# Kernel tuning notes

Hardware: AMD Instinct MI355X
Metric: run time of the kernel (lower is better)

Reference implementation:

```python
import jax, jax.numpy as jnp
import numpy as np

SIM_TIME = 3
ALPHA = 0.9      # membrane decay
RHO = 0.985      # threshold-adaptation decay
BETA_A = 1.8     # adaptation coupling
TH = 1.0         # base threshold
SURR_SCALE = 0.3 # surrogate gradient scale

@jax.custom_vjp
def spike(v):
    return (v > 0.0).astype(v.dtype)

def _spike_fwd(v):
    return spike(v), v

def _spike_bwd(v, g):
    # triangular surrogate gradient
    return (g * SURR_SCALE * jnp.maximum(0.0, 1.0 - jnp.abs(v)),)

spike.defvjp(_spike_fwd, _spike_bwd)

def setup_inputs() -> dict:
    key = jax.random.key(0)
    ks = jax.random.split(key, 6)
    T, B, nin, npre, nad, npost, nout = 32, 128, 512, 1024, 1024, 1024, 256
    s = lambda fan_in: 1.0 / np.sqrt(fan_in)
    return {
        "inp": jax.random.normal(ks[0], (T, B, nin), dtype=jnp.float32),
        "W_pre": jax.random.normal(ks[1], (npre, nin + nad), dtype=jnp.float32) * s(nin + nad),
        "b_pre": jnp.zeros((npre,), jnp.float32),
        "W_ad": jax.random.normal(ks[2], (nad, npre), dtype=jnp.float32) * s(npre),
        "b_ad": jnp.zeros((nad,), jnp.float32),
        "W_post": jax.random.normal(ks[3], (npost, nin + nad), dtype=jnp.float32) * s(nin + nad),
        "b_post": jnp.zeros((npost,), jnp.float32),
        "W_out": jax.random.normal(ks[4], (nout, npost), dtype=jnp.float32) * s(npost),
        "b_out": jnp.zeros((nout,), jnp.float32),
    }

def _rsnn_forward(inp, W_pre, b_pre, W_ad, b_ad, W_post, b_post, W_out, b_out):
    T, B, _ = inp.shape
    nad = W_ad.shape[0]
    npre = W_pre.shape[0]
    npost = W_post.shape[0]
    z = lambda n: jnp.zeros((B, n), inp.dtype)
    # state: (adaptive spikes, v_pre, v_adapt, b_adapt, v_post)
    init = (z(nad), z(npre), z(nad), z(nad), z(npost))

    def step_t(state, inp_t):
        spikes, v_pre, v_a, b_a, v_post = state
        o = None
        for _ in range(SIM_TIME):  # fixed small inner simulation loop
            x = jnp.concatenate([inp_t, spikes], axis=1)            # [B, nin+nad]
            v_pre = ALPHA * v_pre + x @ W_pre.T + b_pre
            s_pre = spike(v_pre - TH)
            v_pre = v_pre - s_pre * TH                               # soft reset
            v_a = ALPHA * v_a + s_pre @ W_ad.T + b_ad
            th_eff = TH + BETA_A * b_a                               # adaptive threshold
            s_a = spike(v_a - th_eff)
            v_a = v_a - s_a * th_eff
            b_a = RHO * b_a + s_a
            spikes = s_a
            x2 = jnp.concatenate([inp_t, s_a], axis=1)
            v_post = ALPHA * v_post + x2 @ W_post.T + b_post
            s_post = spike(v_post - TH)
            v_post = v_post - s_post * TH
            o = s_post @ W_out.T + b_out                             # [B, nout]
        return (spikes, v_pre, v_a, b_a, v_post), o

    final_state, output = jax.lax.scan(step_t, init, inp)            # output [T, B, nout]
    return output, final_state[0]

def reference(inp, W_pre, b_pre, W_ad, b_ad, W_post, b_post, W_out, b_out):
    return _rsnn_forward(inp, W_pre, b_pre, W_ad, b_ad, W_post, b_post, W_out, b_out)
```

## Files before the change

### kernel.cpp

```cpp
#include <hip/hip_runtime.h>

#pragma clang fp contract(off)

typedef unsigned long long u64;
typedef unsigned int u32;

#define ALPHA  0.9f
#define RHO    0.985f
#define BETA_A 1.8f
#define TH     1.0f
#define CAP    (1 << 24)

__global__ __launch_bounds__(256) void transpose_k(const float* __restrict__ src,
                                                   float* __restrict__ dst,
                                                   int R, int C) {
    __shared__ float tile[32][33];
    const int c0 = blockIdx.x * 32;
    const int r0 = blockIdx.y * 32;
    const int tx = threadIdx.x, ty = threadIdx.y;
#pragma unroll
    for (int i = 0; i < 4; ++i)
        tile[ty + i * 8][tx] = src[(r0 + ty + i * 8) * C + c0 + tx];
    __syncthreads();
#pragma unroll
    for (int i = 0; i < 4; ++i)
        dst[(c0 + ty + i * 8) * R + r0 + tx] = tile[tx][ty + i * 8];
}

__global__ __launch_bounds__(256) void ip_gemm(const float* __restrict__ inp,
                                               const float* __restrict__ Wt,
                                               const float* __restrict__ bias,
                                               float* __restrict__ out) {
    __shared__ __align__(16) float s_in[512 * 20];
    const int tid   = threadIdx.x;
    const int chunk = blockIdx.x;
    const int rbase = blockIdx.y * 16;

    for (int idx = tid; idx < 16 * 512; idx += 256) {
        const int r = idx >> 9, k = idx & 511;
        s_in[k * 20 + r] = inp[(rbase + r) * 512 + k];
    }
    __syncthreads();

    const int n = chunk * 256 + tid;
    float acc[16];
#pragma unroll
    for (int r = 0; r < 16; ++r) acc[r] = 0.f;

    for (int k = 0; k < 512; ++k) {
        const float w = Wt[k * 1024 + n];
        const float4* p = (const float4*)(s_in + k * 20);
        const float4 x0 = p[0], x1 = p[1], x2 = p[2], x3 = p[3];
        acc[0]  = fmaf(x0.x, w, acc[0]);  acc[1]  = fmaf(x0.y, w, acc[1]);
        acc[2]  = fmaf(x0.z, w, acc[2]);  acc[3]  = fmaf(x0.w, w, acc[3]);
        acc[4]  = fmaf(x1.x, w, acc[4]);  acc[5]  = fmaf(x1.y, w, acc[5]);
        acc[6]  = fmaf(x1.z, w, acc[6]);  acc[7]  = fmaf(x1.w, w, acc[7]);
        acc[8]  = fmaf(x2.x, w, acc[8]);  acc[9]  = fmaf(x2.y, w, acc[9]);
        acc[10] = fmaf(x2.z, w, acc[10]); acc[11] = fmaf(x2.w, w, acc[11]);
        acc[12] = fmaf(x3.x, w, acc[12]); acc[13] = fmaf(x3.y, w, acc[13]);
        acc[14] = fmaf(x3.z, w, acc[14]); acc[15] = fmaf(x3.w, w, acc[15]);
    }
    const float bn = bias[n];
#pragma unroll
    for (int r = 0; r < 16; ++r) out[(rbase + r) * 1024 + n] = acc[r] + bn;
}

__device__ __forceinline__ u64 ld_u64(const u64* p) {
    return __hip_atomic_load(p, __ATOMIC_RELAXED, __HIP_MEMORY_SCOPE_AGENT);
}
__device__ __forceinline__ void st_u64(u64* p, u64 v) {
    __hip_atomic_store(p, v, __ATOMIC_RELAXED, __HIP_MEMORY_SCOPE_AGENT);
}

__device__ __forceinline__ float gatherseg(const char* __restrict__ Wb,
                                           const int* __restrict__ list,
                                           int i0, int i1, int colB) {
    float a0 = 0.f, a1 = 0.f, a2 = 0.f, a3 = 0.f;
    int i = i0;
    for (; i + 4 <= i1; i += 4) {
        const int4 j = *(const int4*)(list + i);
        a0 += *(const float*)(Wb + (u32)(j.x + colB));
        a1 += *(const float*)(Wb + (u32)(j.y + colB));
        a2 += *(const float*)(Wb + (u32)(j.z + colB));
        a3 += *(const float*)(Wb + (u32)(j.w + colB));
    }
    for (; i < i1; ++i) a0 += *(const float*)(Wb + (u32)(list[i] + colB));
    return (a0 + a1) + (a2 + a3);
}

__device__ __forceinline__ float gather_idx(const float* __restrict__ W,
                                            const int* __restrict__ list, int cnt, int col) {
    float a0 = 0.f, a1 = 0.f, a2 = 0.f, a3 = 0.f;
    int i = 0;
    for (; i + 4 <= cnt; i += 4) {
        const int4 j = *(const int4*)(list + i);
        a0 += W[j.x * 256 + col];
        a1 += W[j.y * 256 + col];
        a2 += W[j.z * 256 + col];
        a3 += W[j.w * 256 + col];
    }
    for (; i < cnt; ++i) a0 += W[list[i] * 256 + col];
    return (a0 + a1) + (a2 + a3);
}

__global__ __launch_bounds__(640) void rsnn_pc(
    const float* __restrict__ Wt_pre,
    const float* __restrict__ Wt_ad,
    const float* __restrict__ Wt_post,
    const float* __restrict__ IP_pre,
    const float* __restrict__ IP_post,
    const float* __restrict__ b_ad_p,
    u64* __restrict__ lines,
    u64* __restrict__ spkO,
    float* __restrict__ out)
{
    const int tid  = threadIdx.x;
    const int bid  = blockIdx.x;
    const int x    = bid & 7;
    const int g    = bid >> 3;
    const int s    = x >> 1;
    const int p    = g * 2 + (x & 1);
    const int wid  = tid >> 6;
    const int lane = tid & 63;

    __shared__ __align__(16) int listP[2][1024];
    __shared__ __align__(16) int listS[2][2][1024];
    __shared__ int cntP_ls[2], cntS_ls[2][2];

    const char* WadB    = (const char*)Wt_ad;
    const char* WpreAB  = (const char*)(Wt_pre  + 512 * 1024);
    const char* WpostAB = (const char*)(Wt_post + 512 * 1024);

    if (wid < 8) {
        const int bi   = tid >> 8;
        const int c    = tid & 255;
        const int col  = s * 256 + c;
        const int b    = 2 * p + bi;
        const int q    = wid & 3;
        const int colB = col * 4;

        float v_pre = 0.f, v_a = 0.f, ba = 0.f, v_post = 0.f, accA = 0.f;
        bool  sa = false;
        const float bad = b_ad_p[col];
        float g1 = 0.f;
        int halfPrev = 0, cntPrev = 0, parPrev = 0;

        for (int e = 1; e <= 96; ++e) {
            const int par = e & 1;
            const int t   = (e - 1) / 3;
            const float ipre = IP_pre[(t * 128 + b) * 1024 + col];
            u64* ln0 = lines + ((p * 2 + par) * 2 + 0) * 64;
            u64* ln1 = lines + ((p * 2 + par) * 2 + 1) * 64;

            v_pre = ALPHA * v_pre + ipre + accA;
            float d = v_pre - TH;
            const bool sp = d > 0.f;
            if (sp) v_pre = d;
            {
                const u64 m = __ballot(sp);
                if (lane == 0) {
                    const u64 eh = ((u64)e) << 32;
                    st_u64(&ln0[(s * 2 + bi) * 8 + 2 * q],     eh | (m & 0xffffffffull));
                    st_u64(&ln0[(s * 2 + bi) * 8 + 2 * q + 1], eh | (m >> 32));
                }
            }
            if (e >= 2)
                g1 = gatherseg(WpostAB, listS[parPrev][bi], 0, halfPrev, colB);
            __syncthreads();

            const int cp = cntP_ls[bi];
            const float accB = gatherseg(WadB, listP[bi], 0, cp, colB);
            v_a = ALPHA * v_a + accB + bad;
            const float th = TH + BETA_A * ba;
            d = v_a - th;
            sa = d > 0.f;
            if (sa) v_a = d;
            ba = RHO * ba + (sa ? 1.f : 0.f);
            {
                const u64 m = __ballot(sa);
                if (lane == 0) {
                    const u64 eh = ((u64)e) << 32;
                    st_u64(&ln1[(s * 2 + bi) * 8 + 2 * q],     eh | (m & 0xffffffffull));
                    st_u64(&ln1[(s * 2 + bi) * 8 + 2 * q + 1], eh | (m >> 32));
                }
            }
            if (e >= 2) {
                const float g2 = gatherseg(WpostAB, listS[parPrev][bi],
                                           halfPrev, cntPrev, colB);
                const int tp = (e - 2) / 3;
                const float ipost = IP_post[(tp * 128 + b) * 1024 + col];
                v_post = ALPHA * v_post + ipost + (g1 + g2);
                float dd = v_post - TH;
                const bool spost = dd > 0.f;
                if (spost) v_post = dd;
                if (e % 3 == 1) {
                    const u64 m = __ballot(spost);
                    if (lane == 0)
                        st_u64(&spkO[(tp * 128 + 2 * p + bi) * 16 + s * 4 + q], m);
                }
            }
            if (e == 96)
                out[32 * 128 * 256 + b * 1024 + col] = sa ? 1.f : 0.f;
            __syncthreads();

            const int cs = cntS_ls[par][bi];
            halfPrev = (cs >> 1) & ~3;
            cntPrev  = cs;
            parPrev  = par;
            if (e < 96)
                accA = gatherseg(WpreAB, listS[par][bi], 0, cs, colB);
        }
        {
            const float ga = gatherseg(WpostAB, listS[0][bi], 0, halfPrev, colB);
            const float gb = gatherseg(WpostAB, listS[0][bi], halfPrev, cntPrev, colB);
            const float ipost = IP_post[(31 * 128 + b) * 1024 + col];
            v_post = ALPHA * v_post + ipost + (ga + gb);
            const float dd = v_post - TH;
            const u64 m = __ballot(dd > 0.f);
            if (lane == 0)
                st_u64(&spkO[(31 * 128 + 2 * p + bi) * 16 + s * 4 + q], m);
        }
    } else if (wid == 8) {
        const int cbi = lane >> 5, r = lane & 31, sl = r >> 3, h = r & 7;
        const int jbase = (sl * 256 + h * 32) << 12;
        for (int e = 1; e <= 96; ++e) {
            const int par = e & 1;
            const u64* ln0 = lines + ((p * 2 + par) * 2 + 0) * 64;
            u64 w; int gd = 0;
            do { w = ld_u64(&ln0[(sl * 2 + cbi) * 8 + h]); }
            while ((w >> 32) != (u64)e && ++gd < CAP);
            const u32 bits = (u32)w;
            const int pc = __popc(bits);
            int incl = pc;
            for (int dlt = 1; dlt < 32; dlt <<= 1) {
                const int v = __shfl_up(incl, dlt, 32);
                if ((lane & 31) >= dlt) incl += v;
            }
            int base = incl - pc;
            u32 m = bits;
            while (m) {
                const int bt = __builtin_ctz(m);
                m &= m - 1;
                listP[cbi][base++] = jbase + (bt << 12);
            }
            if ((lane & 31) == 31) cntP_ls[cbi] = incl;
            __syncthreads();
            __syncthreads();
        }
    } else {
        const int cbi = lane >> 5, r = lane & 31, sl = r >> 3, h = r & 7;
        const int jbase = (sl * 256 + h * 32) << 12;
        for (int e = 1; e <= 96; ++e) {
            const int par = e & 1;
            const u64* ln1 = lines + ((p * 2 + par) * 2 + 1) * 64;
            __syncthreads();
            u64 w; int gd = 0;
            do { w = ld_u64(&ln1[(sl * 2 + cbi) * 8 + h]); }
            while ((w >> 32) != (u64)e && ++gd < CAP);
            const u32 bits = (u32)w;
            const int pc = __popc(bits);
            int incl = pc;
            for (int dlt = 1; dlt < 32; dlt <<= 1) {
                const int v = __shfl_up(incl, dlt, 32);
                if ((lane & 31) >= dlt) incl += v;
            }
            int base = incl - pc;
            u32 m = bits;
            while (m) {
                const int bt = __builtin_ctz(m);
                m &= m - 1;
                listS[par][cbi][base++] = jbase + (bt << 12);
            }
            if ((lane & 31) == 31) cntS_ls[par][cbi] = incl;
            __syncthreads();
        }
    }
}

__global__ __launch_bounds__(256) void out_gemm(const float* __restrict__ Wt_out,
                                                const float* __restrict__ b_out,
                                                const u64* __restrict__ spkO,
                                                float* __restrict__ out) {
    __shared__ u64 bmp[16];
    __shared__ int pc[16];
    __shared__ __align__(16) int list[1024];
    const int r = blockIdx.x, tid = threadIdx.x;
    if (tid < 16) {
        const u64 m = ld_u64(&spkO[r * 16 + tid]);
        bmp[tid] = m;
        pc[tid]  = __popcll(m);
    }
    __syncthreads();
    int total = 0;
#pragma unroll
    for (int w = 0; w < 16; ++w) total += pc[w];
    for (int j = tid; j < 1024; j += 256) {
        const int w = j >> 6, bit = j & 63;
        const u64 m = bmp[w];
        if ((m >> bit) & 1ull) {
            int base = __popcll(m & ((1ull << bit) - 1ull));
            for (int q2 = 0; q2 < w; ++q2) base += pc[q2];
            list[base] = j;
        }
    }
    __syncthreads();
    const float acc = gather_idx(Wt_out, list, total, tid);
    out[r * 256 + tid] = acc + b_out[tid];
}

extern "C" void kernel_launch(void* const* d_in, const int* in_sizes, int n_in,
                              void* d_out, int out_size, void* d_ws, size_t ws_size,
                              hipStream_t stream) {
    (void)in_sizes; (void)n_in; (void)out_size; (void)ws_size;
    const float* inp    = (const float*)d_in[0];
    const float* W_pre  = (const float*)d_in[1];
    const float* b_pre  = (const float*)d_in[2];
    const float* W_ad   = (const float*)d_in[3];
    const float* b_ad   = (const float*)d_in[4];
    const float* W_post = (const float*)d_in[5];
    const float* b_post = (const float*)d_in[6];
    const float* W_out  = (const float*)d_in[7];
    const float* b_out  = (const float*)d_in[8];

    char* base = (char*)d_ws;
    u64*  lines = (u64*)(base + 4096);
    u64*  spkO  = (u64*)(base + 147456);
    float* ws      = (float*)(base + 1048576);
    float* Wt_pre  = ws;
    float* Wt_post = Wt_pre  + 1536 * 1024;
    float* Wt_ad   = Wt_post + 1536 * 1024;
    float* Wt_out  = Wt_ad   + 1024 * 1024;
    float* IP_pre  = Wt_out  + 1024 * 256;
    float* IP_post = IP_pre  + 4096 * 1024;

    hipMemsetAsync(base, 0, 4096 + 131072, stream);

    transpose_k<<<dim3(48, 32), dim3(32, 8), 0, stream>>>(W_pre,  Wt_pre,  1024, 1536);
    transpose_k<<<dim3(48, 32), dim3(32, 8), 0, stream>>>(W_post, Wt_post, 1024, 1536);
    transpose_k<<<dim3(32, 32), dim3(32, 8), 0, stream>>>(W_ad,   Wt_ad,   1024, 1024);
    transpose_k<<<dim3(32, 8),  dim3(32, 8), 0, stream>>>(W_out,  Wt_out,  256,  1024);

    ip_gemm<<<dim3(4, 256), 256, 0, stream>>>(inp, Wt_pre,  b_pre,  IP_pre);
    ip_gemm<<<dim3(4, 256), 256, 0, stream>>>(inp, Wt_post, b_post, IP_post);

    rsnn_pc<<<256, 640, 0, stream>>>(Wt_pre, Wt_ad, Wt_post,
                                     IP_pre, IP_post, b_ad,
                                     lines, spkO, (float*)d_out);

    out_gemm<<<4096, 256, 0, stream>>>(Wt_out, b_out, spkO, (float*)d_out);
}
```

Measured before the change: 1.084 ms.

## Split recurrent kernel to one batch row per block with merged list-builder wave

The persistent recurrent kernel now has each block handle a single batch row instead of two. That doubles the grid to 512 blocks of 320 threads. The two list-builder waves (pre spikes and adaptive spikes) are merged into one wave that handles both stages in sequence. The intent is to spread the gather work over more CUs and shrink per-block shared memory. The cost is a longer serial path in the single builder wave and twice as many spin-polling blocks, which must all be co-resident to avoid deadlock.

```diff
diff --git a/kernel.cpp b/kernel.cpp
--- a/kernel.cpp
+++ b/kernel.cpp
@@ -103,7 +103,7 @@
     return (a0 + a1) + (a2 + a3);
 }
 
-__global__ __launch_bounds__(640) void rsnn_pc(
+__global__ __launch_bounds__(320) void rsnn_pc2(
     const float* __restrict__ Wt_pre,
     const float* __restrict__ Wt_ad,
     const float* __restrict__ Wt_post,
@@ -119,24 +119,24 @@
     const int x    = bid & 7;
     const int g    = bid >> 3;
     const int s    = x >> 1;
-    const int p    = g * 2 + (x & 1);
+    const int b    = g * 2 + (x & 1);
     const int wid  = tid >> 6;
     const int lane = tid & 63;
 
-    __shared__ __align__(16) int listP[2][1024];
-    __shared__ __align__(16) int listS[2][2][1024];
-    __shared__ int cntP_ls[2], cntS_ls[2][2];
+    __shared__ __align__(16) int listP[1024];
+    __shared__ __align__(16) int listS[2][1024];
+    __shared__ int cntP_ls, cntS_ls[2];
 
     const char* WadB    = (const char*)Wt_ad;
     const char* WpreAB  = (const char*)(Wt_pre  + 512 * 1024);
     const char* WpostAB = (const char*)(Wt_post + 512 * 1024);
 
-    if (wid < 8) {
-        const int bi   = tid >> 8;
-        const int c    = tid & 255;
-        const int col  = s * 256 + c;
-        const int b    = 2 * p + bi;
-        const int q    = wid & 3;
+    if (tid == 0) { cntS_ls[0] = 0; cntS_ls[1] = 0; cntP_ls = 0; }
+    __syncthreads();
+
+    if (wid < 4) {
+        const int q    = wid;
+        const int col  = s * 256 + tid;
         const int colB = col * 4;
 
         float v_pre = 0.f, v_a = 0.f, ba = 0.f, v_post = 0.f, accA = 0.f;
@@ -149,8 +149,8 @@
             const int par = e & 1;
             const int t   = (e - 1) / 3;
             const float ipre = IP_pre[(t * 128 + b) * 1024 + col];
-            u64* ln0 = lines + ((p * 2 + par) * 2 + 0) * 64;
-            u64* ln1 = lines + ((p * 2 + par) * 2 + 1) * 64;
+            u64* ln0 = lines + ((b * 2 + par) * 2 + 0) * 32;
+            u64* ln1 = lines + ((b * 2 + par) * 2 + 1) * 32;
 
             v_pre = ALPHA * v_pre + ipre + accA;
             float d = v_pre - TH;
@@ -160,16 +160,16 @@
                 const u64 m = __ballot(sp);
                 if (lane == 0) {
                     const u64 eh = ((u64)e) << 32;
-                    st_u64(&ln0[(s * 2 + bi) * 8 + 2 * q],     eh | (m & 0xffffffffull));
-                    st_u64(&ln0[(s * 2 + bi) * 8 + 2 * q + 1], eh | (m >> 32));
+                    st_u64(&ln0[s * 8 + 2 * q],     eh | (m & 0xffffffffull));
+                    st_u64(&ln0[s * 8 + 2 * q + 1], eh | (m >> 32));
                 }
             }
             if (e >= 2)
-                g1 = gatherseg(WpostAB, listS[parPrev][bi], 0, halfPrev, colB);
+                g1 = gatherseg(WpostAB, listS[parPrev], 0, halfPrev, colB);
             __syncthreads();
 
-            const int cp = cntP_ls[bi];
-            const float accB = gatherseg(WadB, listP[bi], 0, cp, colB);
+            const int cp = cntP_ls;
+            const float accB = gatherseg(WadB, listP, 0, cp, colB);
             v_a = ALPHA * v_a + accB + bad;
             const float th = TH + BETA_A * ba;
             d = v_a - th;
@@ -180,12 +180,12 @@
                 const u64 m = __ballot(sa);
                 if (lane == 0) {
                     const u64 eh = ((u64)e) << 32;
-                    st_u64(&ln1[(s * 2 + bi) * 8 + 2 * q],     eh | (m & 0xffffffffull));
-                    st_u64(&ln1[(s * 2 + bi) * 8 + 2 * q + 1], eh | (m >> 32));
+                    st_u64(&ln1[s * 8 + 2 * q],     eh | (m & 0xffffffffull));
+                    st_u64(&ln1[s * 8 + 2 * q + 1], eh | (m >> 32));
                 }
             }
             if (e >= 2) {
-                const float g2 = gatherseg(WpostAB, listS[parPrev][bi],
+                const float g2 = gatherseg(WpostAB, listS[parPrev],
                                            halfPrev, cntPrev, colB);
                 const int tp = (e - 2) / 3;
                 const float ipost = IP_post[(tp * 128 + b) * 1024 + col];
@@ -196,82 +196,89 @@
                 if (e % 3 == 1) {
                     const u64 m = __ballot(spost);
                     if (lane == 0)
-                        st_u64(&spkO[(tp * 128 + 2 * p + bi) * 16 + s * 4 + q], m);
+                        st_u64(&spkO[(tp * 128 + b) * 16 + s * 4 + q], m);
                 }
             }
             if (e == 96)
                 out[32 * 128 * 256 + b * 1024 + col] = sa ? 1.f : 0.f;
             __syncthreads();
 
-            const int cs = cntS_ls[par][bi];
+            const int cs = cntS_ls[par];
             halfPrev = (cs >> 1) & ~3;
             cntPrev  = cs;
             parPrev  = par;
             if (e < 96)
-                accA = gatherseg(WpreAB, listS[par][bi], 0, cs, colB);
+                accA = gatherseg(WpreAB, listS[par], 0, cs, colB);
         }
         {
-            const float ga = gatherseg(WpostAB, listS[0][bi], 0, halfPrev, colB);
-            const float gb = gatherseg(WpostAB, listS[0][bi], halfPrev, cntPrev, colB);
+            const float ga = gatherseg(WpostAB, listS[0], 0, halfPrev, colB);
+            const float gb = gatherseg(WpostAB, listS[0], halfPrev, cntPrev, colB);
             const float ipost = IP_post[(31 * 128 + b) * 1024 + col];
             v_post = ALPHA * v_post + ipost + (ga + gb);
             const float dd = v_post - TH;
             const u64 m = __ballot(dd > 0.f);
             if (lane == 0)
-                st_u64(&spkO[(31 * 128 + 2 * p + bi) * 16 + s * 4 + q], m);
+                st_u64(&spkO[(31 * 128 + b) * 16 + s * 4 + q], m);
         }
-    } else if (wid == 8) {
-        const int cbi = lane >> 5, r = lane & 31, sl = r >> 3, h = r & 7;
+    } else {
+        const int sl = lane >> 3, h = lane & 7;
+        const bool act = lane < 32;
         const int jbase = (sl * 256 + h * 32) << 12;
         for (int e = 1; e <= 96; ++e) {
             const int par = e & 1;
-            const u64* ln0 = lines + ((p * 2 + par) * 2 + 0) * 64;
-            u64 w; int gd = 0;
-            do { w = ld_u64(&ln0[(sl * 2 + cbi) * 8 + h]); }
-            while ((w >> 32) != (u64)e && ++gd < CAP);
-            const u32 bits = (u32)w;
-            const int pc = __popc(bits);
-            int incl = pc;
-            for (int dlt = 1; dlt < 32; dlt <<= 1) {
-                const int v = __shfl_up(incl, dlt, 32);
-                if ((lane & 31) >= dlt) incl += v;
-            }
-            int base = incl - pc;
-            u32 m = bits;
-            while (m) {
-                const int bt = __builtin_ctz(m);
-                m &= m - 1;
-                listP[cbi][base++] = jbase + (bt << 12);
-            }
-            if ((lane & 31) == 31) cntP_ls[cbi] = incl;
+            const u64* ln0 = lines + ((b * 2 + par) * 2 + 0) * 32;
+            const u64* ln1 = lines + ((b * 2 + par) * 2 + 1) * 32;
+
+            u32 bits = 0;
+            if (act) {
+                u64 w; int gd = 0;
+                do { w = ld_u64(&ln0[sl * 8 + h]); }
+                while ((w >> 32) != (u64)e && ++gd < CAP);
+                bits = (u32)w;
+            }
+            {
+                const int pc = __popc(bits);
+                int incl = pc;
+#pragma unroll
+                for (int dlt = 1; dlt < 32; dlt <<= 1) {
+                    const int v = __shfl_up(incl, dlt, 64);
+                    if (lane >= dlt && lane < 32) incl += v;
+                }
+                int base = incl - pc;
+                u32 m = bits;
+                while (m) {
+                    const int bt = __builtin_ctz(m);
+                    m &= m - 1;
+                    listP[base++] = jbase + (bt << 12);
+                }
+                if (lane == 31) cntP_ls = incl;
+            }
             __syncthreads();
-            __syncthreads();
-        }
-    } else {
-        const int cbi = lane >> 5, r = lane & 31, sl = r >> 3, h = r & 7;
-        const int jbase = (sl * 256 + h * 32) << 12;
-        for (int e = 1; e <= 96; ++e) {
-            const int par = e & 1;
-            const u64* ln1 = lines + ((p * 2 + par) * 2 + 1) * 64;
-            __syncthreads();
-            u64 w; int gd = 0;
-            do { w = ld_u64(&ln1[(sl * 2 + cbi) * 8 + h]); }
-            while ((w >> 32) != (u64)e && ++gd < CAP);
-            const u32 bits = (u32)w;
-            const int pc = __popc(bits);
-            int incl = pc;
-            for (int dlt = 1; dlt < 32; dlt <<= 1) {
-                const int v = __shfl_up(incl, dlt, 32);
-                if ((lane & 31) >= dlt) incl += v;
-            }
-            int base = incl - pc;
-            u32 m = bits;
-            while (m) {
-                const int bt = __builtin_ctz(m);
-                m &= m - 1;
-                listS[par][cbi][base++] = jbase + (bt << 12);
-            }
-            if ((lane & 31) == 31) cntS_ls[par][cbi] = incl;
+
+            bits = 0;
+            if (act) {
+                u64 w; int gd = 0;
+                do { w = ld_u64(&ln1[sl * 8 + h]); }
+                while ((w >> 32) != (u64)e && ++gd < CAP);
+                bits = (u32)w;
+            }
+            {
+                const int pc = __popc(bits);
+                int incl = pc;
+#pragma unroll
+                for (int dlt = 1; dlt < 32; dlt <<= 1) {
+                    const int v = __shfl_up(incl, dlt, 64);
+                    if (lane >= dlt && lane < 32) incl += v;
+                }
+                int base = incl - pc;
+                u32 m = bits;
+                while (m) {
+                    const int bt = __builtin_ctz(m);
+                    m &= m - 1;
+                    listS[par][base++] = jbase + (bt << 12);
+                }
+                if (lane == 31) cntS_ls[par] = incl;
+            }
             __syncthreads();
         }
     }
@@ -324,7 +331,7 @@
 
     char* base = (char*)d_ws;
     u64*  lines = (u64*)(base + 4096);
-    u64*  spkO  = (u64*)(base + 147456);
+    u64*  spkO  = (u64*)(base + 4096 + 131072);
     float* ws      = (float*)(base + 1048576);
     float* Wt_pre  = ws;
     float* Wt_post = Wt_pre  + 1536 * 1024;
@@ -343,9 +350,9 @@
     ip_gemm<<<dim3(4, 256), 256, 0, stream>>>(inp, Wt_pre,  b_pre,  IP_pre);
     ip_gemm<<<dim3(4, 256), 256, 0, stream>>>(inp, Wt_post, b_post, IP_post);
 
-    rsnn_pc<<<256, 640, 0, stream>>>(Wt_pre, Wt_ad, Wt_post,
-                                     IP_pre, IP_post, b_ad,
-                                     lines, spkO, (float*)d_out);
+    rsnn_pc2<<<512, 320, 0, stream>>>(Wt_pre, Wt_ad, Wt_post,
+                                      IP_pre, IP_post, b_ad,
+                                      lines, spkO, (float*)d_out);
 
     out_gemm<<<4096, 256, 0, stream>>>(Wt_out, b_out, spkO, (float*)d_out);
 }
```

New measurement: 1.159 ms. +6.9%, slower.

## Replace producer-consumer list-building warps with per-wave async bitmap polling gathers

Applied to the files above, without the earlier changes.

Removes the dedicated list-building waves and the block-wide __syncthreads in the recurrent kernel. Each compute wave now polls the tagged spike bitmaps itself, from LDS for its own slice and from global memory for other blocks, and walks the set bits to gather weights directly. The W_pre and W_post gathers are fused into one pass over the adaptive spikes. The post-layer update is moved into the same epoch rather than lagging one behind. This trades barrier and list-construction overhead for redundant bitmap decoding in every wave and more polling traffic on global memory.

```diff
diff --git a/kernel.cpp b/kernel.cpp
--- a/kernel.cpp
+++ b/kernel.cpp
@@ -71,21 +71,11 @@
 __device__ __forceinline__ void st_u64(u64* p, u64 v) {
     __hip_atomic_store(p, v, __ATOMIC_RELAXED, __HIP_MEMORY_SCOPE_AGENT);
 }
-
-__device__ __forceinline__ float gatherseg(const char* __restrict__ Wb,
-                                           const int* __restrict__ list,
-                                           int i0, int i1, int colB) {
-    float a0 = 0.f, a1 = 0.f, a2 = 0.f, a3 = 0.f;
-    int i = i0;
-    for (; i + 4 <= i1; i += 4) {
-        const int4 j = *(const int4*)(list + i);
-        a0 += *(const float*)(Wb + (u32)(j.x + colB));
-        a1 += *(const float*)(Wb + (u32)(j.y + colB));
-        a2 += *(const float*)(Wb + (u32)(j.z + colB));
-        a3 += *(const float*)(Wb + (u32)(j.w + colB));
-    }
-    for (; i < i1; ++i) a0 += *(const float*)(Wb + (u32)(list[i] + colB));
-    return (a0 + a1) + (a2 + a3);
+__device__ __forceinline__ u64 ld_lds(const u64* p) {
+    return __hip_atomic_load(p, __ATOMIC_RELAXED, __HIP_MEMORY_SCOPE_WORKGROUP);
+}
+__device__ __forceinline__ void st_lds(u64* p, u64 v) {
+    __hip_atomic_store(p, v, __ATOMIC_RELAXED, __HIP_MEMORY_SCOPE_WORKGROUP);
 }
 
 __device__ __forceinline__ float gather_idx(const float* __restrict__ W,
@@ -103,7 +93,7 @@
     return (a0 + a1) + (a2 + a3);
 }
 
-__global__ __launch_bounds__(640) void rsnn_pc(
+__global__ __launch_bounds__(512) void rsnn_async(
     const float* __restrict__ Wt_pre,
     const float* __restrict__ Wt_ad,
     const float* __restrict__ Wt_post,
@@ -122,158 +112,120 @@
     const int p    = g * 2 + (x & 1);
     const int wid  = tid >> 6;
     const int lane = tid & 63;
-
-    __shared__ __align__(16) int listP[2][1024];
-    __shared__ __align__(16) int listS[2][2][1024];
-    __shared__ int cntP_ls[2], cntS_ls[2][2];
+    const int bi   = wid >> 2;
+    const int q    = wid & 3;
+    const int b    = 2 * p + bi;
+    const int col  = s * 256 + q * 64 + lane;
+    const int colB = col * 4;
+    const u64 M32  = 0xffffffffull;
+
+    __shared__ u64 ltag[2][2][2][8];
+    if (tid < 64) ((u64*)ltag)[tid] = 0;
+    __syncthreads();
 
     const char* WadB    = (const char*)Wt_ad;
     const char* WpreAB  = (const char*)(Wt_pre  + 512 * 1024);
     const char* WpostAB = (const char*)(Wt_post + 512 * 1024);
 
-    if (wid < 8) {
-        const int bi   = tid >> 8;
-        const int c    = tid & 255;
-        const int col  = s * 256 + c;
-        const int b    = 2 * p + bi;
-        const int q    = wid & 3;
-        const int colB = col * 4;
-
-        float v_pre = 0.f, v_a = 0.f, ba = 0.f, v_post = 0.f, accA = 0.f;
-        bool  sa = false;
-        const float bad = b_ad_p[col];
-        float g1 = 0.f;
-        int halfPrev = 0, cntPrev = 0, parPrev = 0;
-
-        for (int e = 1; e <= 96; ++e) {
-            const int par = e & 1;
-            const int t   = (e - 1) / 3;
-            const float ipre = IP_pre[(t * 128 + b) * 1024 + col];
-            u64* ln0 = lines + ((p * 2 + par) * 2 + 0) * 64;
-            u64* ln1 = lines + ((p * 2 + par) * 2 + 1) * 64;
-
-            v_pre = ALPHA * v_pre + ipre + accA;
-            float d = v_pre - TH;
-            const bool sp = d > 0.f;
-            if (sp) v_pre = d;
-            {
-                const u64 m = __ballot(sp);
-                if (lane == 0) {
-                    const u64 eh = ((u64)e) << 32;
-                    st_u64(&ln0[(s * 2 + bi) * 8 + 2 * q],     eh | (m & 0xffffffffull));
-                    st_u64(&ln0[(s * 2 + bi) * 8 + 2 * q + 1], eh | (m >> 32));
-                }
-            }
-            if (e >= 2)
-                g1 = gatherseg(WpostAB, listS[parPrev][bi], 0, halfPrev, colB);
-            __syncthreads();
-
-            const int cp = cntP_ls[bi];
-            const float accB = gatherseg(WadB, listP[bi], 0, cp, colB);
-            v_a = ALPHA * v_a + accB + bad;
-            const float th = TH + BETA_A * ba;
-            d = v_a - th;
-            sa = d > 0.f;
-            if (sa) v_a = d;
-            ba = RHO * ba + (sa ? 1.f : 0.f);
-            {
-                const u64 m = __ballot(sa);
-                if (lane == 0) {
-                    const u64 eh = ((u64)e) << 32;
-                    st_u64(&ln1[(s * 2 + bi) * 8 + 2 * q],     eh | (m & 0xffffffffull));
-                    st_u64(&ln1[(s * 2 + bi) * 8 + 2 * q + 1], eh | (m >> 32));
-                }
-            }
-            if (e >= 2) {
-                const float g2 = gatherseg(WpostAB, listS[parPrev][bi],
-                                           halfPrev, cntPrev, colB);
-                const int tp = (e - 2) / 3;
-                const float ipost = IP_post[(tp * 128 + b) * 1024 + col];
-                v_post = ALPHA * v_post + ipost + (g1 + g2);
-                float dd = v_post - TH;
-                const bool spost = dd > 0.f;
-                if (spost) v_post = dd;
-                if (e % 3 == 1) {
-                    const u64 m = __ballot(spost);
-                    if (lane == 0)
-                        st_u64(&spkO[(tp * 128 + 2 * p + bi) * 16 + s * 4 + q], m);
-                }
-            }
-            if (e == 96)
-                out[32 * 128 * 256 + b * 1024 + col] = sa ? 1.f : 0.f;
-            __syncthreads();
-
-            const int cs = cntS_ls[par][bi];
-            halfPrev = (cs >> 1) & ~3;
-            cntPrev  = cs;
-            parPrev  = par;
-            if (e < 96)
-                accA = gatherseg(WpreAB, listS[par][bi], 0, cs, colB);
-        }
+    float v_pre = 0.f, v_a = 0.f, ba = 0.f, v_post = 0.f, accA = 0.f;
+    bool  sa = false;
+    const float bad = b_ad_p[col];
+    float ipre = 0.f, ipost = 0.f;
+
+    for (int e = 1; e <= 96; ++e) {
+        const int par = e & 1;
+        const u64 tag = ((u64)e) << 32;
+        if ((e - 1) % 3 == 0) {
+            const int t = (e - 1) / 3;
+            ipre  = IP_pre [(t * 128 + b) * 1024 + col];
+            ipost = IP_post[(t * 128 + b) * 1024 + col];
+        }
+        u64* gl0 = lines + ((b * 2 + par) * 2 + 0) * 32;
+        u64* gl1 = lines + ((b * 2 + par) * 2 + 1) * 32;
+
+        v_pre = ALPHA * v_pre + ipre + accA;
+        float d = v_pre - TH;
+        const bool sp = d > 0.f;
+        if (sp) v_pre = d;
         {
-            const float ga = gatherseg(WpostAB, listS[0][bi], 0, halfPrev, colB);
-            const float gb = gatherseg(WpostAB, listS[0][bi], halfPrev, cntPrev, colB);
-            const float ipost = IP_post[(31 * 128 + b) * 1024 + col];
-            v_post = ALPHA * v_post + ipost + (ga + gb);
-            const float dd = v_post - TH;
-            const u64 m = __ballot(dd > 0.f);
+            const u64 m = __ballot(sp);
+            if (lane == 0) {
+                st_u64(&gl0[s * 8 + q * 2],     tag | (m & M32));
+                st_u64(&gl0[s * 8 + q * 2 + 1], tag | (m >> 32));
+                st_lds(&ltag[bi][par][0][q * 2],     tag | (m & M32));
+                st_lds(&ltag[bi][par][0][q * 2 + 1], tag | (m >> 32));
+            }
+        }
+
+        float accB = 0.f;
+        for (int w = 0; w < 32; ++w) {
+            u64 v;
+            if ((w >> 3) == s) {
+                const u64* lp = &ltag[bi][par][0][w & 7];
+                int gd = 0;
+                do { v = ld_lds(lp); } while ((v >> 32) != (u64)e && ++gd < CAP);
+            } else {
+                int gd = 0;
+                do { v = ld_u64(&gl0[w]); } while ((v >> 32) != (u64)e && ++gd < CAP);
+            }
+            u32 bits = (u32)v;
+            const u32 base = ((u32)w) << 17;
+            while (bits) {
+                const int bt = __builtin_ctz(bits);
+                bits &= bits - 1;
+                accB += *(const float*)(WadB + (base + (((u32)bt) << 12) + (u32)colB));
+            }
+        }
+        v_a = ALPHA * v_a + accB + bad;
+        const float th = TH + BETA_A * ba;
+        d = v_a - th;
+        sa = d > 0.f;
+        if (sa) v_a = d;
+        ba = RHO * ba + (sa ? 1.f : 0.f);
+        {
+            const u64 m = __ballot(sa);
+            if (lane == 0) {
+                st_u64(&gl1[s * 8 + q * 2],     tag | (m & M32));
+                st_u64(&gl1[s * 8 + q * 2 + 1], tag | (m >> 32));
+                st_lds(&ltag[bi][par][1][q * 2],     tag | (m & M32));
+                st_lds(&ltag[bi][par][1][q * 2 + 1], tag | (m >> 32));
+            }
+        }
+
+        float accC = 0.f;
+        accA = 0.f;
+        for (int w = 0; w < 32; ++w) {
+            u64 v;
+            if ((w >> 3) == s) {
+                const u64* lp = &ltag[bi][par][1][w & 7];
+                int gd = 0;
+                do { v = ld_lds(lp); } while ((v >> 32) != (u64)e && ++gd < CAP);
+            } else {
+                int gd = 0;
+                do { v = ld_u64(&gl1[w]); } while ((v >> 32) != (u64)e && ++gd < CAP);
+            }
+            u32 bits = (u32)v;
+            const u32 base = ((u32)w) << 17;
+            while (bits) {
+                const int bt = __builtin_ctz(bits);
+                bits &= bits - 1;
+                const u32 off = base + (((u32)bt) << 12) + (u32)colB;
+                accC += *(const float*)(WpostAB + off);
+                accA += *(const float*)(WpreAB  + off);
+            }
+        }
+
+        v_post = ALPHA * v_post + ipost + accC;
+        d = v_post - TH;
+        const bool spost = d > 0.f;
+        if (spost) v_post = d;
+        if (e % 3 == 0) {
+            const u64 m = __ballot(spost);
             if (lane == 0)
-                st_u64(&spkO[(31 * 128 + 2 * p + bi) * 16 + s * 4 + q], m);
-        }
-    } else if (wid == 8) {
-        const int cbi = lane >> 5, r = lane & 31, sl = r >> 3, h = r & 7;
-        const int jbase = (sl * 256 + h * 32) << 12;
-        for (int e = 1; e <= 96; ++e) {
-            const int par = e & 1;
-            const u64* ln0 = lines + ((p * 2 + par) * 2 + 0) * 64;
-            u64 w; int gd = 0;
-            do { w = ld_u64(&ln0[(sl * 2 + cbi) * 8 + h]); }
-            while ((w >> 32) != (u64)e && ++gd < CAP);
-            const u32 bits = (u32)w;
-            const int pc = __popc(bits);
-            int incl = pc;
-            for (int dlt = 1; dlt < 32; dlt <<= 1) {
-                const int v = __shfl_up(incl, dlt, 32);
-                if ((lane & 31) >= dlt) incl += v;
-            }
-            int base = incl - pc;
-            u32 m = bits;
-            while (m) {
-                const int bt = __builtin_ctz(m);
-                m &= m - 1;
-                listP[cbi][base++] = jbase + (bt << 12);
-            }
-            if ((lane & 31) == 31) cntP_ls[cbi] = incl;
-            __syncthreads();
-            __syncthreads();
-        }
-    } else {
-        const int cbi = lane >> 5, r = lane & 31, sl = r >> 3, h = r & 7;
-        const int jbase = (sl * 256 + h * 32) << 12;
-        for (int e = 1; e <= 96; ++e) {
-            const int par = e & 1;
-            const u64* ln1 = lines + ((p * 2 + par) * 2 + 1) * 64;
-            __syncthreads();
-            u64 w; int gd = 0;
-            do { w = ld_u64(&ln1[(sl * 2 + cbi) * 8 + h]); }
-            while ((w >> 32) != (u64)e && ++gd < CAP);
-            const u32 bits = (u32)w;
-            const int pc = __popc(bits);
-            int incl = pc;
-            for (int dlt = 1; dlt < 32; dlt <<= 1) {
-                const int v = __shfl_up(incl, dlt, 32);
-                if ((lane & 31) >= dlt) incl += v;
-            }
-            int base = incl - pc;
-            u32 m = bits;
-            while (m) {
-                const int bt = __builtin_ctz(m);
-                m &= m - 1;
-                listS[par][cbi][base++] = jbase + (bt << 12);
-            }
-            if ((lane & 31) == 31) cntS_ls[par][cbi] = incl;
-            __syncthreads();
-        }
+                st_u64(&spkO[(((e - 1) / 3) * 128 + b) * 16 + s * 4 + q], m);
+        }
+        if (e == 96)
+            out[32 * 128 * 256 + b * 1024 + col] = sa ? 1.f : 0.f;
     }
 }
 
@@ -324,7 +276,7 @@
 
     char* base = (char*)d_ws;
     u64*  lines = (u64*)(base + 4096);
-    u64*  spkO  = (u64*)(base + 147456);
+    u64*  spkO  = (u64*)(base + 4096 + 131072);
     float* ws      = (float*)(base + 1048576);
     float* Wt_pre  = ws;
     float* Wt_post = Wt_pre  + 1536 * 1024;
@@ -343,9 +295,9 @@
     ip_gemm<<<dim3(4, 256), 256, 0, stream>>>(inp, Wt_pre,  b_pre,  IP_pre);
     ip_gemm<<<dim3(4, 256), 256, 0, stream>>>(inp, Wt_post, b_post, IP_post);
 
-    rsnn_pc<<<256, 640, 0, stream>>>(Wt_pre, Wt_ad, Wt_post,
-                                     IP_pre, IP_post, b_ad,
-                                     lines, spkO, (float*)d_out);
+    rsnn_async<<<256, 512, 0, stream>>>(Wt_pre, Wt_ad, Wt_post,
+                                        IP_pre, IP_post, b_ad,
+                                        lines, spkO, (float*)d_out);
 
     out_gemm<<<4096, 256, 0, stream>>>(Wt_out, b_out, spkO, (float*)d_out);
 }
```

Result: slower. 3.090 ms (+185.1%).
